# Performance work log

Hardware: AMD Instinct MI355X
Metric: run time of the kernel (lower is better)

## Reference

```python
import jax, jax.numpy as jnp
import numpy as np

_USRINF = 1e8
K = 16
NUM_PATCHES = 32
ANGLE_THRESHOLD = 1.5708
W_NORMAL = 1.0
W_SURFVAR = 1.0


def _knn_realigned(points, k, invalid_mask=None):
    """k nearest neighbors of each point, re-centered. points [B,N,3] -> [B,N,k,3]."""
    p = jax.lax.stop_gradient(points)  # mirrors points.detach() in distance computation
    d = jnp.sqrt(jnp.sum((p[:, :, None, :] - p[:, None, :, :]) ** 2, axis=-1))  # [B,N,N]
    if invalid_mask is not None:
        d = jnp.where(invalid_mask, _USRINF, d)
    # torch: topk(k, dim=1, largest=False).indices.permute(0,2,1)
    dT = jnp.swapaxes(d, 1, 2)                      # [B, N_query, N_cand]
    _, idx = jax.lax.top_k(-dT, k)                  # [B, N, k] smallest distances
    B = points.shape[0]
    knn = points[jnp.arange(B)[:, None, None], idx]  # [B, N, k, 3]
    return knn - points[:, :, None, :]


def _cov_eig(knn):
    # covariance = knn^T knn per point: [B,N,3,3]
    cov = jnp.einsum('bnki,bnkj->bnij', knn, knn)
    return jnp.linalg.eigh(cov)  # ascending eigenvalues, eigvecs in columns


def _estimate_normal(knn):
    _, vecs = _cov_eig(knn)
    return vecs[..., :, 0]  # eigenvector of smallest eigenvalue, [B,N,3]


def _estimate_surfvar(knn):
    vals, _ = _cov_eig(knn)
    return vals[..., 0] / jnp.sum(vals, axis=-1)  # [B,N]


def _global_invalid_mask(points, gtPoints, gtNormal, angleThreshold):
    p = jax.lax.stop_gradient(points)
    gp = jax.lax.stop_gradient(gtPoints)
    dGT = jnp.sqrt(jnp.sum((p[:, :, None, :] - gp[:, None, :, :]) ** 2, axis=-1))  # [B,N,M]
    nearest = jnp.argmin(dGT, axis=2)  # [B,N]
    B = points.shape[0]
    ideal = gtNormal[jnp.arange(B)[:, None], nearest]  # [B,N,3]
    ang = jnp.einsum('bni,bmi->bnm', ideal, ideal)
    return ang <= jnp.cos(jnp.float32(angleThreshold))


def _patchwise(points, num_patches, k):
    # Patch path: due to the positional-arg bug in the original forward,
    # the patchwise knn runs WITHOUT angle masking.
    B, N, _ = points.shape
    n = N // num_patches
    patches = points.reshape(B * num_patches, n, 3)
    knn = _knn_realigned(patches, k)  # [B*P, n, k, 3]
    normals = _estimate_normal(knn).reshape(B, N, 3)
    surfvar = _estimate_surfvar(knn).reshape(B, N)
    return normals, surfvar


def setup_inputs() -> dict:
    key = jax.random.key(0)
    k1, k2, k3 = jax.random.split(key, 3)
    pointCloud = jax.random.normal(k1, (2, 8192, 3), dtype=jnp.float32)
    gtPoints = jax.random.normal(k2, (2, 8192, 3), dtype=jnp.float32)
    gn = jax.random.normal(k3, (2, 8192, 3), dtype=jnp.float32)
    gtNormal = gn / jnp.linalg.norm(gn, axis=2, keepdims=True)
    return {"pointCloud": pointCloud, "gtPoints": gtPoints, "gtNormal": gtNormal}


def reference(pointCloud, gtPoints, gtNormal):
    invalid = _global_invalid_mask(pointCloud, gtPoints, gtNormal, ANGLE_THRESHOLD)
    knn_global = _knn_realigned(pointCloud, K, invalid)  # [B,N,k,3]

    normal_global = _estimate_normal(knn_global)  # [B,N,3]
    normal_patch, surfvar_patch = _patchwise(pointCloud, NUM_PATCHES, K)

    # normalLossAbs=True branch
    normal_loss = jnp.mean(
        jnp.linalg.norm(jnp.abs(normal_patch) - jnp.abs(normal_global), axis=2)
    )[None] * W_NORMAL

    surfvar_global = _estimate_surfvar(knn_global)  # [B,N]
    surfvar_loss = jnp.mean((surfvar_patch - surfvar_global) ** 2)[None] * W_SURFVAR

    return (normal_loss, surfvar_loss, normal_global)
```

## Files before the change

### kernel.cpp

```cpp
#include <hip/hip_runtime.h>
#include <hip/hip_bf16.h>
#include <float.h>
#include <limits.h>

#define NPTS 8192
#define NB 2
#define NQ (NB * NPTS)
#define KNN 16
#define NPATCHES 64


__device__ __forceinline__ float f_sign(float a, float b) {
    float aa = fabsf(a);
    return (b >= 0.0f) ? aa : -aa;
}

__device__ __forceinline__ float slapy2f(float x, float y) {
#pragma clang fp contract(off)
    float xa = fabsf(x), ya = fabsf(y);
    float w = fmaxf(xa, ya), z = fminf(xa, ya);
    if (z == 0.0f) return w;
    float q = z / w;
    return w * sqrtf(1.0f + q * q);
}

__device__ __forceinline__ void slartgf(float f, float g, float* cs, float* sn, float* r) {
#pragma clang fp contract(off)
    if (g == 0.0f) { *cs = 1.0f; *sn = 0.0f; *r = f; }
    else if (f == 0.0f) { *cs = 0.0f; *sn = (g >= 0.0f) ? 1.0f : -1.0f; *r = fabsf(g); }
    else {
        float d = sqrtf(f * f + g * g);
        *cs = fabsf(f) / d;
        float rr = f_sign(d, f);
        *sn = g / rr;
        *r = rr;
    }
}

__device__ void slaev2f(float a, float b, float c, float* rt1, float* rt2,
                        float* cs1, float* sn1) {
#pragma clang fp contract(off)
    float sm = a + c, df = a - c;
    float adf = fabsf(df);
    float tb = b + b;
    float ab = fabsf(tb);
    float acmx, acmn;
    if (fabsf(a) > fabsf(c)) { acmx = a; acmn = c; } else { acmx = c; acmn = a; }
    float rt;
    if (adf > ab)      { float q = ab / adf; rt = adf * sqrtf(1.0f + q * q); }
    else if (adf < ab) { float q = adf / ab; rt = ab * sqrtf(1.0f + q * q); }
    else               { rt = ab * sqrtf(2.0f); }
    int sgn1;
    if (sm < 0.0f) {
        *rt1 = 0.5f * (sm - rt); sgn1 = -1;
        *rt2 = (acmx / *rt1) * acmn - (b / *rt1) * b;
    } else if (sm > 0.0f) {
        *rt1 = 0.5f * (sm + rt); sgn1 = 1;
        *rt2 = (acmx / *rt1) * acmn - (b / *rt1) * b;
    } else {
        *rt1 = 0.5f * rt; *rt2 = -0.5f * rt; sgn1 = 1;
    }
    float cs; int sgn2;
    if (df >= 0.0f) { cs = df + rt; sgn2 = 1; } else { cs = df - rt; sgn2 = -1; }
    float acs = fabsf(cs);
    if (acs > ab) {
        float ct = -tb / cs;
        *sn1 = 1.0f / sqrtf(1.0f + ct * ct);
        *cs1 = ct * (*sn1);
    } else {
        if (ab == 0.0f) { *cs1 = 1.0f; *sn1 = 0.0f; }
        else {
            float tn = -cs / tb;
            *cs1 = 1.0f / sqrtf(1.0f + tn * tn);
            *sn1 = tn * (*cs1);
        }
    }
    if (sgn1 == sgn2) { float tn = *cs1; *cs1 = -(*sn1); *sn1 = tn; }
}

__device__ void eigh3_lapack(const float cov[6], float* W, float evals[3], float nvec[3]) {
#pragma clang fp contract(off)
    const float eps = 5.9604644775390625e-08f;
    const float eps2 = eps * eps;
    const float safmin = 1.1754943508222875e-38f;
#define D_(i)  W[(i)]
#define E_(i)  W[4 + (i)]
#define WC_(i) W[8 + (i)]
#define WS_(i) W[12 + (i)]
#define ZZ(r, cf) W[16 + ((cf) - 1) * 3 + (r)]
    float a00 = cov[0], a10 = cov[1], a11 = cov[2], a20 = cov[3], a21 = cov[4], a22 = cov[5];

    float tau, v2, beta;
    {
        float alpha = a10;
        float xnorm = fabsf(a20);
        if (xnorm == 0.0f) { tau = 0.0f; v2 = 0.0f; beta = alpha; }
        else {
            beta = -f_sign(slapy2f(alpha, xnorm), alpha);
            tau = (beta - alpha) / beta;
            v2 = a20 * (1.0f / (alpha - beta));
            float p0 = tau * a11 + tau * (a21 * v2);
            float p1 = tau * a21 + (tau * v2) * a22;
            float al = -0.5f * tau * (p0 + p1 * v2);
            float w0 = p0 + al;
            float w1 = p1 + al * v2;
            a11 = (a11 - w0) - w0;
            a21 = (a21 - v2 * w0) - w1;
            a22 = (a22 - v2 * w1) - w1 * v2;
        }
    }
    D_(1) = a00; D_(2) = a11; D_(3) = a22;
    E_(1) = beta; E_(2) = a21;
    for (int cf = 1; cf <= 3; ++cf)
        for (int r0 = 0; r0 < 3; ++r0)
            ZZ(r0, cf) = (r0 == cf - 1) ? 1.0f : 0.0f;

    const int n = 3;
    int nmaxit = n * 30, jtot = 0, l1 = 1;
    int l, m, lsv, lend, lendsv;
    float p, g, r, c, s, f, b;

L10:
    if (l1 > n) goto L160;
    if (l1 > 1) E_(l1 - 1) = 0.0f;
    m = n;
    if (l1 <= n - 1) {
        for (int mi = l1; mi <= n - 1; ++mi) {
            float tst = fabsf(E_(mi));
            if (tst == 0.0f) { m = mi; goto L30; }
            if (tst <= (sqrtf(fabsf(D_(mi))) * sqrtf(fabsf(D_(mi + 1)))) * eps) {
                E_(mi) = 0.0f; m = mi; goto L30;
            }
        }
        m = n;
    }
L30:
    l = l1; lsv = l; lend = m; lendsv = lend; l1 = m + 1;
    if (lend == l) goto L10;
    {
        float anorm = fabsf(D_(lend));
        for (int i2 = l; i2 <= lend - 1; ++i2) {
            anorm = fmaxf(anorm, fabsf(D_(i2)));
            anorm = fmaxf(anorm, fabsf(E_(i2)));
        }
        if (anorm == 0.0f) goto L10;
    }
    if (fabsf(D_(lend)) < fabsf(D_(l))) { lend = lsv; l = lendsv; }
    if (lend > l) goto L40;
    goto L90;

L40:
    if (l != lend) {
        m = lend;
        for (int mi = l; mi <= lend - 1; ++mi) {
            float tst = fabsf(E_(mi)); tst = tst * tst;
            if (tst <= (eps2 * fabsf(D_(mi))) * fabsf(D_(mi + 1)) + safmin) { m = mi; goto L60; }
        }
    } else { m = lend; }
L60:
    if (m < lend) E_(m) = 0.0f;
    p = D_(l);
    if (m == l) goto L80;
    if (m == l + 1) {
        float rt1, rt2, c2, s2;
        slaev2f(D_(l), E_(l), D_(l + 1), &rt1, &rt2, &c2, &s2);
        for (int r2 = 0; r2 < 3; ++r2) {
            float temp = ZZ(r2, l + 1);
            ZZ(r2, l + 1) = c2 * temp - s2 * ZZ(r2, l);
            ZZ(r2, l)     = s2 * temp + c2 * ZZ(r2, l);
        }
        D_(l) = rt1; D_(l + 1) = rt2; E_(l) = 0.0f;
        l += 2;
        if (l <= lend) goto L40;
        goto L140;
    }
    if (jtot == nmaxit) goto L140;
    jtot++;
    g = (D_(l + 1) - p) / (2.0f * E_(l));
    r = slapy2f(g, 1.0f);
    g = D_(m) - p + (E_(l) / (g + f_sign(r, g)));
    s = 1.0f; c = 1.0f; p = 0.0f;
    for (int i2 = m - 1; i2 >= l; --i2) {
        f = s * E_(i2); b = c * E_(i2);
        slartgf(g, f, &c, &s, &r);
        if (i2 != m - 1) E_(i2 + 1) = r;
        g = D_(i2 + 1) - p;
        r = (D_(i2) - g) * s + 2.0f * c * b;
        p = s * r;
        D_(i2 + 1) = g + p;
        g = c * r - b;
        WC_(i2) = c; WS_(i2) = -s;
    }
    {
        int mm = m - l + 1;
        for (int J = mm - 1; J >= 1; --J) {
            float ct = WC_(l + J - 1), st = WS_(l + J - 1);
            for (int r2 = 0; r2 < 3; ++r2) {
                float temp = ZZ(r2, l + J);
                ZZ(r2, l + J)     = ct * temp - st * ZZ(r2, l + J - 1);
                ZZ(r2, l + J - 1) = st * temp + ct * ZZ(r2, l + J - 1);
            }
        }
    }
    D_(l) = D_(l) - p;
    E_(l) = g;
    goto L40;
L80:
    D_(l) = p;
    l++;
    if (l <= lend) goto L40;
    goto L140;

L90:
    if (l != lend) {
        m = lend;
        for (int mi = l; mi >= lend + 1; --mi) {
            float tst = fabsf(E_(mi - 1)); tst = tst * tst;
            if (tst <= (eps2 * fabsf(D_(mi))) * fabsf(D_(mi - 1)) + safmin) { m = mi; goto L110; }
        }
    } else { m = lend; }
L110:
    if (m > lend) E_(m - 1) = 0.0f;
    p = D_(l);
    if (m == l) goto L130;
    if (m == l - 1) {
        float rt1, rt2, c2, s2;
        slaev2f(D_(l - 1), E_(l - 1), D_(l), &rt1, &rt2, &c2, &s2);
        for (int r2 = 0; r2 < 3; ++r2) {
            float temp = ZZ(r2, l);
            ZZ(r2, l)     = c2 * temp - s2 * ZZ(r2, l - 1);
            ZZ(r2, l - 1) = s2 * temp + c2 * ZZ(r2, l - 1);
        }
        D_(l - 1) = rt1; D_(l) = rt2; E_(l - 1) = 0.0f;
        l -= 2;
        if (l >= lend) goto L90;
        goto L140;
    }
    if (jtot == nmaxit) goto L140;
    jtot++;
    g = (D_(l - 1) - p) / (2.0f * E_(l - 1));
    r = slapy2f(g, 1.0f);
    g = D_(m) - p + (E_(l - 1) / (g + f_sign(r, g)));
    s = 1.0f; c = 1.0f; p = 0.0f;
    for (int i2 = m; i2 <= l - 1; ++i2) {
        f = s * E_(i2); b = c * E_(i2);
        slartgf(g, f, &c, &s, &r);
        if (i2 != m) E_(i2 - 1) = r;
        g = D_(i2) - p;
        r = (D_(i2 + 1) - g) * s + 2.0f * c * b;
        p = s * r;
        D_(i2) = g + p;
        g = c * r - b;
        WC_(i2) = c; WS_(i2) = s;
    }
    {
        int mm = l - m + 1;
        for (int J = 1; J <= mm - 1; ++J) {
            float ct = WC_(m + J - 1), st = WS_(m + J - 1);
            for (int r2 = 0; r2 < 3; ++r2) {
                float temp = ZZ(r2, m + J);
                ZZ(r2, m + J)     = ct * temp - st * ZZ(r2, m + J - 1);
                ZZ(r2, m + J - 1) = st * temp + ct * ZZ(r2, m + J - 1);
            }
        }
    }
    D_(l) = D_(l) - p;
    E_(l - 1) = g;
    goto L90;
L130:
    D_(l) = p;
    l--;
    if (l >= lend) goto L90;
    goto L140;

L140:
    if (jtot < nmaxit) goto L10;
    goto L190;

L160:
    for (int ii = 2; ii <= n; ++ii) {
        int i2 = ii - 1, k2 = i2;
        p = D_(i2);
        for (int j2 = ii; j2 <= n; ++j2)
            if (D_(j2) < p) { k2 = j2; p = D_(j2); }
        if (k2 != i2) {
            D_(k2) = D_(i2); D_(i2) = p;
            for (int r2 = 0; r2 < 3; ++r2) {
                float t = ZZ(r2, i2); ZZ(r2, i2) = ZZ(r2, k2); ZZ(r2, k2) = t;
            }
        }
    }
L190:
    if (tau != 0.0f) {
        for (int cf = 1; cf <= 3; ++cf) {
            float wv = ZZ(1, cf) + v2 * ZZ(2, cf);
            float tw = tau * wv;
            ZZ(1, cf) = ZZ(1, cf) - tw;
            ZZ(2, cf) = ZZ(2, cf) - v2 * tw;
        }
    }
    evals[0] = D_(1); evals[1] = D_(2); evals[2] = D_(3);
    nvec[0] = ZZ(0, 1); nvec[1] = ZZ(1, 1); nvec[2] = ZZ(2, 1);
#undef D_
#undef E_
#undef WC_
#undef WS_
#undef ZZ
}


typedef unsigned long long u64;

__device__ __forceinline__ u64 packKey(float d, int j) {
    return ((u64)__float_as_uint(d) << 32) | (unsigned int)j;
}

__device__ __forceinline__ u64 shflxor_u64(u64 v, int s) {
    unsigned int lo = (unsigned int)v;
    unsigned int hi = (unsigned int)(v >> 32);
    lo = __shfl_xor(lo, s);
    hi = __shfl_xor(hi, s);
    return ((u64)hi << 32) | lo;
}

__device__ __forceinline__ void csw(u64& a, u64& b) {
    bool sw = b < a;
    u64 t = sw ? b : a;
    b = sw ? a : b;
    a = t;
}

__device__ __forceinline__ void insert16(u64 (&bd)[16], u64 key) {
    if (key >= bd[15]) return;
    bd[15] = key;
#pragma unroll
    for (int k = 15; k >= 1; --k) {
        if (bd[k] < bd[k - 1]) { u64 t = bd[k]; bd[k] = bd[k - 1]; bd[k - 1] = t; }
    }
}

__device__ __forceinline__ void bitonic16(u64 (&bd)[16]) {
#pragma unroll
    for (int d = 8; d >= 1; d >>= 1) {
#pragma unroll
        for (int k = 0; k < 16; ++k) {
            if ((k & d) == 0) csw(bd[k], bd[k + d]);
        }
    }
}

__device__ __forceinline__ void sort8(u64 (&v)[8]) {
    csw(v[0], v[1]); csw(v[2], v[3]); csw(v[0], v[2]); csw(v[1], v[3]); csw(v[1], v[2]);
    csw(v[4], v[5]); csw(v[6], v[7]); csw(v[4], v[6]); csw(v[5], v[7]); csw(v[5], v[6]);
    csw(v[0], v[4]); csw(v[1], v[5]); csw(v[2], v[6]); csw(v[3], v[7]);
    csw(v[2], v[4]); csw(v[3], v[5]);
    csw(v[1], v[2]); csw(v[3], v[4]); csw(v[5], v[6]);
}

__device__ __forceinline__ void merge8into16(u64 (&bd)[16], u64 (&key)[8]) {
#pragma unroll
    for (int j = 0; j < 8; ++j) {
        u64 o = key[7 - j];
        bd[8 + j] = (o < bd[8 + j]) ? o : bd[8 + j];
    }
    bitonic16(bd);
}

__device__ __forceinline__ void mergeTree(u64 (&bd)[16], int sub, int s) {
    bool active = ((sub & (2 * s - 1)) == 0);
#pragma unroll
    for (int k = 0; k < 16; ++k) {
        u64 od = shflxor_u64(bd[15 - k], s);
        bool take = active && (od < bd[k]);
        bd[k] = take ? od : bd[k];
    }
    bitonic16(bd);
}


__global__ void __launch_bounds__(256, 4) kNearestGT(
        const float* __restrict__ pts, const float* __restrict__ gtP,
        const float* __restrict__ gtN, float* __restrict__ idealW) {
#pragma clang fp contract(off)
    __shared__ float4 tile[256];
    int tid = threadIdx.x;
    int sub = tid & 15;
    int qL = tid >> 4;
    int qrow = blockIdx.x * 16 + qL;
    int b = qrow >> 13, bbase = b << 13;
    float px = pts[qrow * 3 + 0], py = pts[qrow * 3 + 1], pz = pts[qrow * 3 + 2];
    float dm = FLT_MAX; int im = INT_MAX;
    for (int t = 0; t < NPTS / 256; ++t) {
        int crow = bbase + t * 256 + tid;
        tile[tid] = make_float4(gtP[crow * 3 + 0], gtP[crow * 3 + 1], gtP[crow * 3 + 2], 0.f);
        __syncthreads();
        for (int cj = sub; cj < 256; cj += 16) {
            float4 cpt = tile[cj];
            float dx = px - cpt.x;
            float dy = py - cpt.y;
            float dz = pz - cpt.z;
            float d = sqrtf(dx * dx + dy * dy + dz * dz);
            int j = t * 256 + cj;
            if (d < dm || (d == dm && j < im)) { dm = d; im = j; }
        }
        __syncthreads();
    }
#pragma unroll
    for (int s = 1; s < 16; s <<= 1) {
        float od = __shfl_xor(dm, s);
        int   oi = __shfl_xor(im, s);
        bool take = (od < dm) || (od == dm && oi < im);
        dm = take ? od : dm;
        im = take ? oi : im;
    }
    if (sub == 0) {
        int src = bbase + im;
        idealW[qrow * 3 + 0] = gtN[src * 3 + 0];
        idealW[qrow * 3 + 1] = gtN[src * 3 + 1];
        idealW[qrow * 3 + 2] = gtN[src * 3 + 2];
    }
}

__global__ void __launch_bounds__(256, 4) kGlobalKNN(
        const float* __restrict__ pts, const float* __restrict__ idealW,
        int* __restrict__ idxG) {
#pragma clang fp contract(off)
    __shared__ float4 sp[256];
    __shared__ float4 si[256];
    int tid = threadIdx.x;
    int sub = tid & 31;
    int qL = tid >> 5;
    int qrow = blockIdx.x * 8 + qL;
    int b = qrow >> 13, bbase = b << 13;
    float px = pts[qrow * 3 + 0], py = pts[qrow * 3 + 1], pz = pts[qrow * 3 + 2];
    float ix = idealW[qrow * 3 + 0], iy = idealW[qrow * 3 + 1], iz = idealW[qrow * 3 + 2];
    const float cthr = -3.6199900765e-06f;
    u64 bd[16];
#pragma unroll
    for (int k = 0; k < 16; ++k) bd[k] = ~0ull;
    for (int t = 0; t < NPTS / 256; ++t) {
        int crow = bbase + t * 256 + tid;
        sp[tid] = make_float4(pts[crow * 3 + 0], pts[crow * 3 + 1], pts[crow * 3 + 2], 0.f);
        si[tid] = make_float4(idealW[crow * 3 + 0], idealW[crow * 3 + 1], idealW[crow * 3 + 2], 0.f);
        __syncthreads();
        u64 key[8];
#pragma unroll
        for (int i = 0; i < 8; ++i) {
            int cj = sub + 32 * i;
            float4 cpt = sp[cj];
            float4 cnr = si[cj];
            float dx = cpt.x - px;
            float dy = cpt.y - py;
            float dz = cpt.z - pz;
            float d = sqrtf(dx * dx + dy * dy + dz * dz);
            float dot = fmaf(iz, cnr.z, fmaf(iy, cnr.y, ix * cnr.x));
            if (dot <= cthr) d = 1.0e8f;
            key[i] = packKey(d, t * 256 + cj);
        }
        sort8(key);
        merge8into16(bd, key);
        __syncthreads();
    }
    mergeTree(bd, sub, 1);
    mergeTree(bd, sub, 2);
    mergeTree(bd, sub, 4);
    mergeTree(bd, sub, 8);
    mergeTree(bd, sub, 16);
    if (sub == 0) {
#pragma unroll
        for (int k = 0; k < 16; ++k)
            idxG[qrow * KNN + k] = bbase + (int)(bd[k] & 0xffffffffu);
    }
}

__global__ void __launch_bounds__(256, 4) kPatchKNN(
        const float* __restrict__ pts, int* __restrict__ idxP) {
#pragma clang fp contract(off)
    __shared__ float4 sp[256];
    int tid = threadIdx.x;
    int sub = tid & 3;
    int qL = tid >> 2;
    int qrow = blockIdx.x * 64 + qL;
    int pbase = (qrow >> 8) << 8;
    int crow = pbase + tid;
    sp[tid] = make_float4(pts[crow * 3 + 0], pts[crow * 3 + 1], pts[crow * 3 + 2], 0.f);
    __syncthreads();
    float px = pts[qrow * 3 + 0], py = pts[qrow * 3 + 1], pz = pts[qrow * 3 + 2];
    u64 bd[16];
#pragma unroll
    for (int k = 0; k < 16; ++k) bd[k] = ~0ull;
    for (int cj = sub; cj < 256; cj += 4) {
        float4 cpt = sp[cj];
        float dx = cpt.x - px;
        float dy = cpt.y - py;
        float dz = cpt.z - pz;
        float d = sqrtf(dx * dx + dy * dy + dz * dz);
        insert16(bd, packKey(d, cj));
    }
    mergeTree(bd, sub, 1);
    mergeTree(bd, sub, 2);
    if (sub == 0) {
#pragma unroll
        for (int k = 0; k < 16; ++k)
            idxP[qrow * KNN + k] = pbase + (int)(bd[k] & 0xffffffffu);
    }
}

__global__ void __launch_bounds__(256) kEigen(
        const float* __restrict__ pts,
        const int* __restrict__ idxG, const int* __restrict__ idxP,
        float* __restrict__ outNormG, float* __restrict__ svG,
        float* __restrict__ normP, float* __restrict__ svP) {
#pragma clang fp contract(off)
    __shared__ float Wall[256 * 27];
    int tid = threadIdx.x;
    int t = blockIdx.x * 256 + tid;
    int isG = (t < NQ) ? 1 : 0;
    int q = isG ? t : (t - NQ);
    const int* idxArr = isG ? idxG : idxP;
    float cx = pts[q * 3 + 0], cy = pts[q * 3 + 1], cz = pts[q * 3 + 2];
    float c00 = 0.f, c10 = 0.f, c11 = 0.f, c20 = 0.f, c21 = 0.f, c22 = 0.f;
    for (int k = 0; k < KNN; ++k) {
        int nb = idxArr[q * KNN + k];
        float vx = pts[nb * 3 + 0] - cx;
        float vy = pts[nb * 3 + 1] - cy;
        float vz = pts[nb * 3 + 2] - cz;
        c00 = fmaf(vx, vx, c00);
        c10 = fmaf(vy, vx, c10);
        c11 = fmaf(vy, vy, c11);
        c20 = fmaf(vz, vx, c20);
        c21 = fmaf(vz, vy, c21);
        c22 = fmaf(vz, vz, c22);
    }
    float cov[6] = {c00, c10, c11, c20, c21, c22};
    float evals[3], nv[3];
    eigh3_lapack(cov, &Wall[tid * 27], evals, nv);
    float sv = evals[0] / ((evals[0] + evals[1]) + evals[2]);
    if (isG) {
        outNormG[q * 3 + 0] = nv[0];
        outNormG[q * 3 + 1] = nv[1];
        outNormG[q * 3 + 2] = nv[2];
        svG[q] = sv;
    } else {
        normP[q * 3 + 0] = nv[0];
        normP[q * 3 + 1] = nv[1];
        normP[q * 3 + 2] = nv[2];
        svP[q] = sv;
    }
}

__global__ void __launch_bounds__(256) kLoss(
        const float* __restrict__ normP, const float* __restrict__ svP,
        const float* __restrict__ svG, const float* __restrict__ normG,
        float* __restrict__ out) {
#pragma clang fp contract(off)
    __shared__ double sA[256];
    __shared__ double sB[256];
    int tid = threadIdx.x;
    double accN = 0.0, accS = 0.0;
    for (int q = tid; q < NQ; q += 256) {
        float ax = fabsf(normP[q * 3 + 0]) - fabsf(normG[q * 3 + 0]);
        float ay = fabsf(normP[q * 3 + 1]) - fabsf(normG[q * 3 + 1]);
        float az = fabsf(normP[q * 3 + 2]) - fabsf(normG[q * 3 + 2]);
        accN += (double)sqrtf(ax * ax + ay * ay + az * az);
        float ds = svP[q] - svG[q];
        accS += (double)(ds * ds);
    }
    sA[tid] = accN; sB[tid] = accS;
    __syncthreads();
    for (int s2 = 128; s2 > 0; s2 >>= 1) {
        if (tid < s2) { sA[tid] += sA[tid + s2]; sB[tid] += sB[tid + s2]; }
        __syncthreads();
    }
    if (tid == 0) {
        out[0] = (float)(sA[0] / (double)NQ);
        out[1] = (float)(sB[0] / (double)NQ);
    }
}

extern "C" void kernel_launch(void* const* d_in, const int* in_sizes, int n_in,
                              void* d_out, int out_size, void* d_ws, size_t ws_size,
                              hipStream_t stream) {
    const float* pts = (const float*)d_in[0];
    const float* gtP = (const float*)d_in[1];
    const float* gtN = (const float*)d_in[2];
    float* out = (float*)d_out;
    float* ws = (float*)d_ws;

    float* idealW = ws;
    int* idxG = (int*)(ws + NQ * 3);
    int* idxP = idxG + NQ * KNN;
    float* normP = (float*)(idxP + NQ * KNN);
    float* svG = normP + NQ * 3;
    float* svP = svG + NQ;
    float* outNormG = out + 2;

    kNearestGT<<<dim3(NQ / 16), dim3(256), 0, stream>>>(pts, gtP, gtN, idealW);
    kGlobalKNN<<<dim3(NQ / 8), dim3(256), 0, stream>>>(pts, idealW, idxG);
    kPatchKNN<<<dim3(NQ / 64), dim3(256), 0, stream>>>(pts, idxP);
    kEigen<<<dim3(2 * NQ / 256), dim3(256), 0, stream>>>(pts, idxG, idxP,
                                                         outNormG, svG, normP, svP);
    kLoss<<<dim3(1), dim3(256), 0, stream>>>(normP, svP, svG, outNormG, out);
}
```

Measured before the change: 477.1 us.

## Fuse nearest-GT and patch KNN into one launch with wider splits

Merges the nearest-ground-truth search and the patch KNN into one kernel, with block ranges choosing the role, which removes one launch and lets the two independent jobs overlap on the device. The nearest-GT search now gives each query 32 lanes instead of 16, with an unrolled, branch-free loop. The patch KNN now uses 8 lanes per query and a batched sort8+merge instead of a per-candidate insertion sort, plus an extra merge stage. The eigen kernel moves to 64-thread blocks to spread its work over more blocks. The costs are more shuffle merges and a larger grid for the nearest-GT part.

```diff
diff --git a/kernel.cpp b/kernel.cpp
--- a/kernel.cpp
+++ b/kernel.cpp
@@ -330,15 +330,6 @@
     a = t;
 }
 
-__device__ __forceinline__ void insert16(u64 (&bd)[16], u64 key) {
-    if (key >= bd[15]) return;
-    bd[15] = key;
-#pragma unroll
-    for (int k = 15; k >= 1; --k) {
-        if (bd[k] < bd[k - 1]) { u64 t = bd[k]; bd[k] = bd[k - 1]; bd[k - 1] = t; }
-    }
-}
-
 __device__ __forceinline__ void bitonic16(u64 (&bd)[16]) {
 #pragma unroll
     for (int d = 8; d >= 1; d >>= 1) {
@@ -378,46 +369,89 @@
 }
 
 
-__global__ void __launch_bounds__(256, 4) kNearestGT(
+__global__ void __launch_bounds__(256, 4) kAux(
         const float* __restrict__ pts, const float* __restrict__ gtP,
-        const float* __restrict__ gtN, float* __restrict__ idealW) {
-#pragma clang fp contract(off)
-    __shared__ float4 tile[256];
+        const float* __restrict__ gtN, float* __restrict__ idealW,
+        int* __restrict__ idxP) {
+#pragma clang fp contract(off)
+    __shared__ float4 shb[256];
     int tid = threadIdx.x;
-    int sub = tid & 15;
-    int qL = tid >> 4;
-    int qrow = blockIdx.x * 16 + qL;
-    int b = qrow >> 13, bbase = b << 13;
-    float px = pts[qrow * 3 + 0], py = pts[qrow * 3 + 1], pz = pts[qrow * 3 + 2];
-    float dm = FLT_MAX; int im = INT_MAX;
-    for (int t = 0; t < NPTS / 256; ++t) {
-        int crow = bbase + t * 256 + tid;
-        tile[tid] = make_float4(gtP[crow * 3 + 0], gtP[crow * 3 + 1], gtP[crow * 3 + 2], 0.f);
+    if (blockIdx.x < NQ / 8) {
+        int sub = tid & 31;
+        int qL = tid >> 5;
+        int qrow = blockIdx.x * 8 + qL;
+        int b = qrow >> 13, bbase = b << 13;
+        float px = pts[qrow * 3 + 0], py = pts[qrow * 3 + 1], pz = pts[qrow * 3 + 2];
+        float dm = FLT_MAX; int im = INT_MAX;
+        for (int t = 0; t < NPTS / 256; ++t) {
+            int crow = bbase + t * 256 + tid;
+            shb[tid] = make_float4(gtP[crow * 3 + 0], gtP[crow * 3 + 1], gtP[crow * 3 + 2], 0.f);
+            __syncthreads();
+#pragma unroll
+            for (int i = 0; i < 8; ++i) {
+                int cj = sub + 32 * i;
+                float4 cpt = shb[cj];
+                float dx = px - cpt.x;
+                float dy = py - cpt.y;
+                float dz = pz - cpt.z;
+                float d = sqrtf(dx * dx + dy * dy + dz * dz);
+                int j = t * 256 + cj;
+                bool take = (d < dm) || (d == dm && j < im);
+                dm = take ? d : dm;
+                im = take ? j : im;
+            }
+            __syncthreads();
+        }
+#pragma unroll
+        for (int s = 1; s < 32; s <<= 1) {
+            float od = __shfl_xor(dm, s);
+            int   oi = __shfl_xor(im, s);
+            bool take = (od < dm) || (od == dm && oi < im);
+            dm = take ? od : dm;
+            im = take ? oi : im;
+        }
+        if (sub == 0) {
+            int src = bbase + im;
+            idealW[qrow * 3 + 0] = gtN[src * 3 + 0];
+            idealW[qrow * 3 + 1] = gtN[src * 3 + 1];
+            idealW[qrow * 3 + 2] = gtN[src * 3 + 2];
+        }
+    } else {
+        int pb = blockIdx.x - NQ / 8;
+        int sub = tid & 7;
+        int qL = tid >> 3;
+        int qrow = pb * 32 + qL;
+        int pbase = ((pb * 32) >> 8) << 8;
+        int crow = pbase + tid;
+        shb[tid] = make_float4(pts[crow * 3 + 0], pts[crow * 3 + 1], pts[crow * 3 + 2], 0.f);
         __syncthreads();
-        for (int cj = sub; cj < 256; cj += 16) {
-            float4 cpt = tile[cj];
-            float dx = px - cpt.x;
-            float dy = py - cpt.y;
-            float dz = pz - cpt.z;
-            float d = sqrtf(dx * dx + dy * dy + dz * dz);
-            int j = t * 256 + cj;
-            if (d < dm || (d == dm && j < im)) { dm = d; im = j; }
-        }
-        __syncthreads();
-    }
-#pragma unroll
-    for (int s = 1; s < 16; s <<= 1) {
-        float od = __shfl_xor(dm, s);
-        int   oi = __shfl_xor(im, s);
-        bool take = (od < dm) || (od == dm && oi < im);
-        dm = take ? od : dm;
-        im = take ? oi : im;
-    }
-    if (sub == 0) {
-        int src = bbase + im;
-        idealW[qrow * 3 + 0] = gtN[src * 3 + 0];
-        idealW[qrow * 3 + 1] = gtN[src * 3 + 1];
-        idealW[qrow * 3 + 2] = gtN[src * 3 + 2];
+        float px = pts[qrow * 3 + 0], py = pts[qrow * 3 + 1], pz = pts[qrow * 3 + 2];
+        u64 bd[16];
+#pragma unroll
+        for (int k = 0; k < 16; ++k) bd[k] = ~0ull;
+        for (int batch = 0; batch < 4; ++batch) {
+            u64 key[8];
+#pragma unroll
+            for (int i = 0; i < 8; ++i) {
+                int cj = sub + 64 * batch + 8 * i;
+                float4 cpt = shb[cj];
+                float dx = cpt.x - px;
+                float dy = cpt.y - py;
+                float dz = cpt.z - pz;
+                float d = sqrtf(dx * dx + dy * dy + dz * dz);
+                key[i] = packKey(d, cj);
+            }
+            sort8(key);
+            merge8into16(bd, key);
+        }
+        mergeTree(bd, sub, 1);
+        mergeTree(bd, sub, 2);
+        mergeTree(bd, sub, 4);
+        if (sub == 0) {
+#pragma unroll
+            for (int k = 0; k < 16; ++k)
+                idxP[qrow * KNN + k] = pbase + (int)(bd[k] & 0xffffffffu);
+        }
     }
 }
 
@@ -473,48 +507,15 @@
     }
 }
 
-__global__ void __launch_bounds__(256, 4) kPatchKNN(
-        const float* __restrict__ pts, int* __restrict__ idxP) {
-#pragma clang fp contract(off)
-    __shared__ float4 sp[256];
-    int tid = threadIdx.x;
-    int sub = tid & 3;
-    int qL = tid >> 2;
-    int qrow = blockIdx.x * 64 + qL;
-    int pbase = (qrow >> 8) << 8;
-    int crow = pbase + tid;
-    sp[tid] = make_float4(pts[crow * 3 + 0], pts[crow * 3 + 1], pts[crow * 3 + 2], 0.f);
-    __syncthreads();
-    float px = pts[qrow * 3 + 0], py = pts[qrow * 3 + 1], pz = pts[qrow * 3 + 2];
-    u64 bd[16];
-#pragma unroll
-    for (int k = 0; k < 16; ++k) bd[k] = ~0ull;
-    for (int cj = sub; cj < 256; cj += 4) {
-        float4 cpt = sp[cj];
-        float dx = cpt.x - px;
-        float dy = cpt.y - py;
-        float dz = cpt.z - pz;
-        float d = sqrtf(dx * dx + dy * dy + dz * dz);
-        insert16(bd, packKey(d, cj));
-    }
-    mergeTree(bd, sub, 1);
-    mergeTree(bd, sub, 2);
-    if (sub == 0) {
-#pragma unroll
-        for (int k = 0; k < 16; ++k)
-            idxP[qrow * KNN + k] = pbase + (int)(bd[k] & 0xffffffffu);
-    }
-}
-
-__global__ void __launch_bounds__(256) kEigen(
+__global__ void __launch_bounds__(64) kEigen(
         const float* __restrict__ pts,
         const int* __restrict__ idxG, const int* __restrict__ idxP,
         float* __restrict__ outNormG, float* __restrict__ svG,
         float* __restrict__ normP, float* __restrict__ svP) {
 #pragma clang fp contract(off)
-    __shared__ float Wall[256 * 27];
+    __shared__ float Wall[64 * 27];
     int tid = threadIdx.x;
-    int t = blockIdx.x * 256 + tid;
+    int t = blockIdx.x * 64 + tid;
     int isG = (t < NQ) ? 1 : 0;
     int q = isG ? t : (t - NQ);
     const int* idxArr = isG ? idxG : idxP;
@@ -595,10 +596,9 @@
     float* svP = svG + NQ;
     float* outNormG = out + 2;
 
-    kNearestGT<<<dim3(NQ / 16), dim3(256), 0, stream>>>(pts, gtP, gtN, idealW);
+    kAux<<<dim3(NQ / 8 + NQ / 32), dim3(256), 0, stream>>>(pts, gtP, gtN, idealW, idxP);
     kGlobalKNN<<<dim3(NQ / 8), dim3(256), 0, stream>>>(pts, idealW, idxG);
-    kPatchKNN<<<dim3(NQ / 64), dim3(256), 0, stream>>>(pts, idxP);
-    kEigen<<<dim3(2 * NQ / 256), dim3(256), 0, stream>>>(pts, idxG, idxP,
-                                                         outNormG, svG, normP, svP);
+    kEigen<<<dim3(2 * NQ / 64), dim3(64), 0, stream>>>(pts, idxG, idxP,
+                                                       outNormG, svG, normP, svP);
     kLoss<<<dim3(1), dim3(256), 0, stream>>>(normP, svP, svG, outNormG, out);
 }
```

New measurement: 405.0 us. 1.18x faster.
